# Kernel optimization log

Hardware: AMD Instinct MI355X
Metric: run time of the kernel (lower is better)

Reference implementation:

```python
import jax, jax.numpy as jnp
import numpy as np

N = 50000      # nodes
E = 400000     # edges (avg degree 8)
IN = 512       # in_dim
HID = 512      # hid
NUM_RSU = 1000 # batch==0 nodes; equals max(batch)+1 so cat() row counts match


def setup_inputs() -> dict:
    key = jax.random.key(0)
    ks = jax.random.split(key, 5)
    x = jax.random.normal(ks[0], (N, IN), jnp.float32)
    edge_index = jax.random.randint(ks[1], (2, E), 0, N, jnp.int32)
    # sorted graph ids: first NUM_RSU nodes are RSU (batch 0), rest split into 999 vehicle graphs
    n_veh = N - NUM_RSU
    veh_batch = 1 + (jnp.arange(n_veh) * (NUM_RSU - 1)) // n_veh
    batch = jnp.concatenate([jnp.zeros(NUM_RSU, jnp.int32), veh_batch.astype(jnp.int32)])
    W1 = jax.random.normal(ks[2], (IN, HID), jnp.float32) * (1.0 / np.sqrt(IN))
    b1 = jnp.zeros((HID,), jnp.float32)
    W2 = jax.random.normal(ks[3], (HID, HID), jnp.float32) * (1.0 / np.sqrt(HID))
    b2 = jnp.zeros((HID,), jnp.float32)
    return {"x": x, "edge_index": edge_index, "batch": batch,
            "W1": W1, "b1": b1, "W2": W2, "b2": b2, "num_rsu": NUM_RSU}


def reference(x, edge_index, batch, W1, b1, W2, b2, num_rsu):
    n = x.shape[0]
    loop = jnp.arange(n, dtype=edge_index.dtype)
    src = jnp.concatenate([edge_index[0], loop])  # self-loops appended (GCNConv default)
    dst = jnp.concatenate([edge_index[1], loop])
    # symmetric normalization D^{-1/2} (A+I) D^{-1/2}
    deg = jax.ops.segment_sum(jnp.ones_like(dst, jnp.float32), dst, num_segments=n)
    dinv = jnp.where(deg > 0, jax.lax.rsqrt(deg), 0.0)
    norm = dinv[src] * dinv[dst]  # [E+N]

    def gcn(h, W, b):
        m = (h @ W)[src] * norm[:, None]                       # gather + scale
        return jax.ops.segment_sum(m, dst, num_segments=n) + b # scatter-add

    h = jax.nn.relu(gcn(x, W1, b1))
    h = gcn(h, W2, b2)

    rsu = h[:num_rsu]                 # batch == 0 nodes (sorted layout)
    veh = h[num_rsu:]
    seg = batch[num_rsu:]             # values 1..num_rsu-1
    s = jax.ops.segment_sum(veh, seg, num_segments=num_rsu)
    cnt = jax.ops.segment_sum(jnp.ones_like(seg, jnp.float32), seg, num_segments=num_rsu)
    veh_pool = s / jnp.maximum(cnt, 1.0)[:, None]  # mean pool; empty segment 0 stays zero
    return jnp.concatenate([rsu, veh_pool], axis=-1)
```

## Files before the change

### kernel.cpp

```cpp
#include <hip/hip_runtime.h>

#define N_NODES 50000
#define E_EDGES 400000
#define DIM     512
#define NRSU    1000
#define NVEH    (N_NODES - NRSU)
#define NB_SCAN 196

typedef __attribute__((ext_vector_type(8))) __bf16 bf16x8;
typedef __attribute__((ext_vector_type(4))) float  f32x4;
typedef __attribute__((ext_vector_type(8))) unsigned short ush8v;

__device__ __forceinline__ unsigned short f2bf_rne(float x) {
    unsigned u = __float_as_uint(x);
    unsigned r = u + 0x7fff + ((u >> 16) & 1);
    return (unsigned short)(r >> 16);
}
__device__ __forceinline__ float bf2f(unsigned short b) {
    return __uint_as_float((unsigned)b << 16);
}
__device__ __forceinline__ void split1(float v, unsigned short& h, unsigned short& l) {
    h = f2bf_rne(v);
    l = f2bf_rne(v - bf2f(h));
}
__device__ __forceinline__ void cvt8(uint4 v, float* f) {
    f[0] = __uint_as_float(v.x << 16); f[1] = __uint_as_float(v.x & 0xffff0000u);
    f[2] = __uint_as_float(v.y << 16); f[3] = __uint_as_float(v.y & 0xffff0000u);
    f[4] = __uint_as_float(v.z << 16); f[5] = __uint_as_float(v.z & 0xffff0000u);
    f[6] = __uint_as_float(v.w << 16); f[7] = __uint_as_float(v.w & 0xffff0000u);
}

typedef __attribute__((address_space(1))) const unsigned char ga_u8;
typedef __attribute__((address_space(3))) unsigned char la_u8;
__device__ __forceinline__ void gload16(const void* g, void* l) {
    __builtin_amdgcn_global_load_lds((ga_u8*)g, (la_u8*)l, 16, 0, 0);
}

__global__ void k_zero_int(int* __restrict__ p, int n) {
    int i = blockIdx.x * 256 + threadIdx.x;
    if (i < n) p[i] = 0;
}

__global__ void k_tobf16(const float* __restrict__ in, unsigned short* __restrict__ out) {
    size_t i = ((size_t)blockIdx.x * 256 + threadIdx.x) * 8;
    float4 a = *reinterpret_cast<const float4*>(in + i);
    float4 b = *reinterpret_cast<const float4*>(in + i + 4);
    ush8v o;
    o[0] = f2bf_rne(a.x); o[1] = f2bf_rne(a.y); o[2] = f2bf_rne(a.z); o[3] = f2bf_rne(a.w);
    o[4] = f2bf_rne(b.x); o[5] = f2bf_rne(b.y); o[6] = f2bf_rne(b.z); o[7] = f2bf_rne(b.w);
    *reinterpret_cast<ush8v*>(out + i) = o;
}

__global__ void k_count(const int* __restrict__ dst, int* __restrict__ cnt) {
    int e = blockIdx.x * 256 + threadIdx.x;
    if (e < E_EDGES) atomicAdd(&cnt[dst[e]], 1);
}

__global__ __launch_bounds__(256) void k_scan1(const int* __restrict__ cnt,
                                               int* __restrict__ rowptr,
                                               int* __restrict__ bsum) {
    __shared__ int sh[256];
    int tid = threadIdx.x;
    int i = blockIdx.x * 256 + tid;
    int v = (i < N_NODES) ? cnt[i] : 0;
    sh[tid] = v;
    __syncthreads();
    #pragma unroll
    for (int off = 1; off < 256; off <<= 1) {
        int t = (tid >= off) ? sh[tid - off] : 0;
        __syncthreads();
        sh[tid] += t;
        __syncthreads();
    }
    if (i < N_NODES) rowptr[i] = sh[tid] - v;
    if (tid == 255) bsum[blockIdx.x] = sh[255];
}

__global__ __launch_bounds__(256) void k_scan2(int* __restrict__ bsum) {
    __shared__ int sh[256];
    int tid = threadIdx.x;
    int v = (tid < NB_SCAN) ? bsum[tid] : 0;
    sh[tid] = v;
    __syncthreads();
    #pragma unroll
    for (int off = 1; off < 256; off <<= 1) {
        int t = (tid >= off) ? sh[tid - off] : 0;
        __syncthreads();
        sh[tid] += t;
        __syncthreads();
    }
    if (tid < NB_SCAN) bsum[tid] = sh[tid] - v;
}

__global__ void k_scan3(int* __restrict__ rowptr, const int* __restrict__ bsum,
                        int* __restrict__ cntfill, float* __restrict__ dinv) {
    int i = blockIdx.x * 256 + threadIdx.x;
    if (i < N_NODES) {
        rowptr[i] += bsum[blockIdx.x];
        int c = cntfill[i];
        dinv[i] = rsqrtf((float)c + 1.0f);
        cntfill[i] = 0;
    }
    if (i == 0) rowptr[N_NODES] = E_EDGES;
}

__global__ void k_fill(const int* __restrict__ ei, const int* __restrict__ rowptr,
                       int* __restrict__ fill, int* __restrict__ col,
                       const float* __restrict__ dinv, float* __restrict__ wnorm) {
    int e = blockIdx.x * 256 + threadIdx.x;
    if (e >= E_EDGES) return;
    int s = ei[e];
    int d = ei[E_EDGES + e];
    int p = atomicAdd(&fill[d], 1);
    int idx = rowptr[d] + p;
    col[idx] = s;
    wnorm[idx] = dinv[s] * dinv[d];
}

__global__ void k_segbounds(const int* __restrict__ batch, int* __restrict__ seg) {
    int v = blockIdx.x * 256 + threadIdx.x;
    if (v >= NVEH) return;
    int b = batch[NRSU + v];
    if (v == 0) {
        for (int s = 0; s <= b; ++s) seg[s] = 0;
    } else {
        int bp = batch[NRSU + v - 1];
        for (int s = bp + 1; s <= b; ++s) seg[s] = v;
    }
    if (v == NVEH - 1) {
        for (int s = b + 1; s <= NRSU; ++s) seg[s] = NVEH;
    }
}

__global__ void k_wsplit(const float* __restrict__ W1, const float* __restrict__ W2,
                         unsigned short* __restrict__ W1h, unsigned short* __restrict__ W1l,
                         unsigned short* __restrict__ W2h, unsigned short* __restrict__ W2l) {
    const float* W = blockIdx.y ? W2 : W1;
    unsigned short* Wh = blockIdx.y ? W2h : W1h;
    unsigned short* Wl = blockIdx.y ? W2l : W1l;
    int n = blockIdx.x;
    for (int k = threadIdx.x; k < DIM; k += 256) {
        float v = W[(size_t)k * DIM + n];
        unsigned short h, l;
        split1(v, h, l);
        Wh[(size_t)n * DIM + k] = h;
        Wl[(size_t)n * DIM + k] = l;
    }
}

template<int MODE>
__global__ __launch_bounds__(256) void k_gemm_mfma(const unsigned short* __restrict__ Ab,
                                                   const unsigned short* __restrict__ BhT,
                                                   const unsigned short* __restrict__ BlT,
                                                   float* __restrict__ C,
                                                   unsigned short* __restrict__ Cb, int M,
                                                   const float* __restrict__ bias,
                                                   const float* __restrict__ bscale) {
    const int BM = 128, BN = 128, BK = 32;
    __shared__ unsigned short sA [BM * BK];
    __shared__ unsigned short sBh[BN * BK];
    __shared__ unsigned short sBl[BN * BK];

    int tid = threadIdx.x;
    int wv = tid >> 6;
    int ln = tid & 63;

    int wgid;
    if (MODE == 2) {
        const int q = 195, r = 4;
        int id = blockIdx.x;
        int xcd = id & 7, idx = id >> 3;
        wgid = (xcd < r ? xcd * (q + 1) : r * (q + 1) + (xcd - r) * q) + idx;
    } else {
        wgid = blockIdx.x;
    }
    int col0 = (wgid & 3) * BN;
    int row0 = (wgid >> 2) * BM;

    int wr = wv >> 1, wc = wv & 1;
    int fr = ln & 15;
    int ks16 = ln >> 4;

    f32x4 zero = {0.f, 0.f, 0.f, 0.f};
    f32x4 acc[4][4];
    #pragma unroll
    for (int m = 0; m < 4; ++m)
        #pragma unroll
        for (int n = 0; n < 4; ++n) acc[m][n] = zero;

    for (int k0 = 0; k0 < DIM; k0 += BK) {
        __syncthreads();
        #pragma unroll
        for (int p = 0; p < 2; ++p) {
            int idx = p * 256 + tid;
            int r = idx >> 2;
            int slot = idx & 3;
            int c = ((slot ^ ((r >> 1) & 3)) << 3);
            int arow = row0 + r; if (arow > M - 1) arow = M - 1;
            size_t aoff = (size_t)arow * DIM + k0 + c;
            size_t boff = (size_t)(col0 + r) * DIM + k0 + c;
            int lbyte = p * 4096 + wv * 1024;
            gload16(Ab + aoff, (char*)sA + lbyte);
            gload16(BhT + boff, (char*)sBh + lbyte);
            gload16(BlT + boff, (char*)sBl + lbyte);
        }
        __syncthreads();

        bf16x8 a[4], bh[4], bl[4];
        #pragma unroll
        for (int m = 0; m < 4; ++m) {
            int r = wr * 64 + m * 16 + fr;
            int e = r * BK + ((ks16 ^ ((r >> 1) & 3)) << 3);
            a[m] = *reinterpret_cast<const bf16x8*>(&sA[e]);
        }
        #pragma unroll
        for (int n = 0; n < 4; ++n) {
            int r = wc * 64 + n * 16 + fr;
            int e = r * BK + ((ks16 ^ ((r >> 1) & 3)) << 3);
            bh[n] = *reinterpret_cast<const bf16x8*>(&sBh[e]);
            bl[n] = *reinterpret_cast<const bf16x8*>(&sBl[e]);
        }
        #pragma unroll
        for (int m = 0; m < 4; ++m)
            #pragma unroll
            for (int n = 0; n < 4; ++n) {
                acc[m][n] = __builtin_amdgcn_mfma_f32_16x16x32_bf16(a[m], bh[n], acc[m][n], 0, 0, 0);
                acc[m][n] = __builtin_amdgcn_mfma_f32_16x16x32_bf16(a[m], bl[n], acc[m][n], 0, 0, 0);
            }
    }

    int rbase = row0 + wr * 64 + (ln >> 4) * 4;
    int cbase = col0 + wc * 64 + (ln & 15);
    #pragma unroll
    for (int m = 0; m < 4; ++m)
        #pragma unroll
        for (int r4 = 0; r4 < 4; ++r4) {
            int row = rbase + m * 16 + r4;
            if (row < M) {
                if (MODE == 2) {
                    #pragma unroll
                    for (int n = 0; n < 4; ++n) {
                        int cc = cbase + n * 16;
                        Cb[(size_t)row * DIM + cc] =
                            f2bf_rne(fmaxf(acc[m][n][r4] + bias[cc], 0.f));
                    }
                } else {
                    float bs = bscale[row];
                    float* dst = (row < NRSU) ? (C + (size_t)row * 1024)
                                              : (C + (size_t)(row - NRSU) * 1024 + 512);
                    #pragma unroll
                    for (int n = 0; n < 4; ++n) {
                        int cc = cbase + n * 16;
                        dst[cc] = acc[m][n][r4] + bias[cc] * bs;
                    }
                }
            }
        }
}

__global__ __launch_bounds__(256) void k_gather_bf(const int* __restrict__ rowptr,
                                                   const int* __restrict__ col,
                                                   const float* __restrict__ wnorm,
                                                   const float* __restrict__ dinv,
                                                   const unsigned short* __restrict__ pre,
                                                   unsigned short* __restrict__ ob) {
    int node = blockIdx.x * 4 + (threadIdx.x >> 6);
    if (node >= N_NODES) return;
    int lane = threadIdx.x & 63;
    int c = lane * 8;

    float di = dinv[node];
    float w0 = di * di;
    float s[8], t[8];
    {
        uint4 sv = *reinterpret_cast<const uint4*>(pre + (size_t)node * DIM + c);
        float fa[8]; cvt8(sv, fa);
        #pragma unroll
        for (int i = 0; i < 8; ++i) { s[i] = w0 * fa[i]; t[i] = 0.f; }
    }

    int beg = rowptr[node], end = rowptr[node + 1];
    int deg = end - beg;
    for (int j0 = 0; j0 < deg; j0 += 64) {
        int j = j0 + lane;
        int cj = 0; float wj = 0.f;
        if (j < deg) { cj = col[beg + j]; wj = wnorm[beg + j]; }
        int lim = deg - j0; if (lim > 64) lim = 64;
        for (int jj = 0; jj < lim; jj += 8) {
            int sidx[8]; float sw[8];
            #pragma unroll
            for (int q = 0; q < 8; ++q) {
                sidx[q] = __shfl(cj, jj + q);
                sw[q]   = __shfl(wj, jj + q);
            }
            uint4 v[8];
            #pragma unroll
            for (int q = 0; q < 8; ++q)
                v[q] = *reinterpret_cast<const uint4*>(pre + (size_t)sidx[q] * DIM + c);
            #pragma unroll
            for (int q = 0; q < 8; ++q) {
                float f[8]; cvt8(v[q], f);
                if ((q & 1) == 0) {
                    #pragma unroll
                    for (int i = 0; i < 8; ++i) s[i] = fmaf(sw[q], f[i], s[i]);
                } else {
                    #pragma unroll
                    for (int i = 0; i < 8; ++i) t[i] = fmaf(sw[q], f[i], t[i]);
                }
            }
        }
    }
    ush8v h;
    #pragma unroll
    for (int i = 0; i < 8; ++i) h[i] = f2bf_rne(s[i] + t[i]);
    *reinterpret_cast<ush8v*>(ob + (size_t)node * DIM + c) = h;
}

__global__ __launch_bounds__(64) void k_pool_sp(const unsigned short* __restrict__ A2b,
                                                const int* __restrict__ seg,
                                                unsigned short* __restrict__ SPb,
                                                float* __restrict__ bscale) {
    int s = blockIdx.x;
    int c = threadIdx.x * 8;
    {
        uint4 v = *reinterpret_cast<const uint4*>(A2b + (size_t)s * DIM + c);
        *reinterpret_cast<uint4*>(SPb + (size_t)s * DIM + c) = v;
    }
    int beg = seg[s], end = seg[s + 1];
    float acc[8] = {0.f, 0.f, 0.f, 0.f, 0.f, 0.f, 0.f, 0.f};
    for (int v = beg; v < end; ++v) {
        uint4 t = *reinterpret_cast<const uint4*>(A2b + (size_t)(NRSU + v) * DIM + c);
        float f[8]; cvt8(t, f);
        #pragma unroll
        for (int i = 0; i < 8; ++i) acc[i] += f[i];
    }
    float inv = 1.0f / fmaxf((float)(end - beg), 1.0f);
    ush8v h;
    #pragma unroll
    for (int i = 0; i < 8; ++i) h[i] = f2bf_rne(acc[i] * inv);
    *reinterpret_cast<ush8v*>(SPb + (size_t)(NRSU + s) * DIM + c) = h;
    if (threadIdx.x == 0) {
        bscale[s] = 1.0f;
        bscale[NRSU + s] = (end > beg) ? 1.0f : 0.0f;
    }
}

extern "C" void kernel_launch(void* const* d_in, const int* in_sizes, int n_in,
                              void* d_out, int out_size, void* d_ws, size_t ws_size,
                              hipStream_t stream) {
    const float* x     = (const float*)d_in[0];
    const int*   ei    = (const int*)d_in[1];
    const int*   batch = (const int*)d_in[2];
    const float* W1    = (const float*)d_in[3];
    const float* b1    = (const float*)d_in[4];
    const float* W2    = (const float*)d_in[5];
    const float* b2    = (const float*)d_in[6];
    float* out = (float*)d_out;

    char* ws = (char*)d_ws;
    const size_t HALF = (size_t)N_NODES * DIM * 2;
    unsigned short* Axb = (unsigned short*)(ws);
    unsigned short* A2b = (unsigned short*)(ws);
    unsigned short* h1b = (unsigned short*)(ws + 2 * HALF);
    unsigned short* xb  = (unsigned short*)(ws + 3 * HALF);
    char* p = ws + 4 * HALF;
    float* dinv    = (float*)p;                p += (size_t)N_NODES * 4;
    int*   cnt     = (int*)p;                  p += (size_t)N_NODES * 4;
    int*   rowptr  = (int*)p;                  p += (size_t)(N_NODES + 4) * 4;
    int*   col     = (int*)p;                  p += (size_t)E_EDGES * 4;
    float* wnorm   = (float*)p;                p += (size_t)E_EDGES * 4;
    int*   bsum    = (int*)p;                  p += 1024;
    int*   seg     = (int*)p;                  p += (size_t)(NRSU + 8) * 4;
    unsigned short* SPb = (unsigned short*)p;  p += (size_t)2 * NRSU * DIM * 2;
    float* bscale  = (float*)p;                p += (size_t)2 * NRSU * 4;
    unsigned short* W1h = (unsigned short*)p;  p += (size_t)DIM * DIM * 2;
    unsigned short* W1l = (unsigned short*)p;  p += (size_t)DIM * DIM * 2;
    unsigned short* W2h = (unsigned short*)p;  p += (size_t)DIM * DIM * 2;
    unsigned short* W2l = (unsigned short*)p;  p += (size_t)DIM * DIM * 2;

    dim3 blk(256);
    const int gN = (N_NODES + 255) / 256;
    const int gE = (E_EDGES + 255) / 256;
    const int gV = (NVEH + 255) / 256;

    k_zero_int <<<gN, blk, 0, stream>>>(cnt, N_NODES);
    k_count    <<<gE, blk, 0, stream>>>(ei + E_EDGES, cnt);
    k_scan1    <<<gN, blk, 0, stream>>>(cnt, rowptr, bsum);
    k_scan2    <<<1,  blk, 0, stream>>>(bsum);
    k_scan3    <<<gN, blk, 0, stream>>>(rowptr, bsum, cnt, dinv);
    k_fill     <<<gE, blk, 0, stream>>>(ei, rowptr, cnt, col, dinv, wnorm);
    k_segbounds<<<gV, blk, 0, stream>>>(batch, seg);
    k_wsplit   <<<dim3(DIM, 2), blk, 0, stream>>>(W1, W2, W1h, W1l, W2h, W2l);
    k_tobf16   <<<(int)((size_t)N_NODES * DIM / 8 / 256), blk, 0, stream>>>(x, xb);

    k_gather_bf<<<(N_NODES + 3) / 4, blk, 0, stream>>>(rowptr, col, wnorm, dinv, xb, Axb);
    const int NWG1 = ((N_NODES + 127) / 128) * 4;
    k_gemm_mfma<2><<<NWG1, blk, 0, stream>>>(Axb, W1h, W1l, nullptr, h1b, N_NODES, b1, nullptr);

    k_gather_bf<<<(N_NODES + 3) / 4, blk, 0, stream>>>(rowptr, col, wnorm, dinv, h1b, A2b);
    k_pool_sp<<<NRSU, dim3(64), 0, stream>>>(A2b, seg, SPb, bscale);
    const int NWG2 = ((2 * NRSU + 127) / 128) * 4;
    k_gemm_mfma<1><<<NWG2, blk, 0, stream>>>(SPb, W2h, W2l, out, nullptr, 2 * NRSU, b2, bscale);
}
```

Baseline: 354.8 us.

## Load GEMM MFMA operands directly from global memory instead of staging through LDS

The bf16 split-precision GEMM no longer stages A and B tiles into shared memory with global_load_lds and barriers. Each lane now reads its MFMA fragments straight from global memory through precomputed row pointers, and the k-loop is unrolled by 4. This removes the two __syncthreads per k-step and the LDS round trip. In exchange, operands are no longer shared across waves, so each wave re-reads tiles from global or L2 memory, and the loads are strided 16-byte reads that coalesce less well.

```diff
diff --git a/kernel.cpp b/kernel.cpp
--- a/kernel.cpp
+++ b/kernel.cpp
@@ -28,12 +28,6 @@
     f[2] = __uint_as_float(v.y << 16); f[3] = __uint_as_float(v.y & 0xffff0000u);
     f[4] = __uint_as_float(v.z << 16); f[5] = __uint_as_float(v.z & 0xffff0000u);
     f[6] = __uint_as_float(v.w << 16); f[7] = __uint_as_float(v.w & 0xffff0000u);
-}
-
-typedef __attribute__((address_space(1))) const unsigned char ga_u8;
-typedef __attribute__((address_space(3))) unsigned char la_u8;
-__device__ __forceinline__ void gload16(const void* g, void* l) {
-    __builtin_amdgcn_global_load_lds((ga_u8*)g, (la_u8*)l, 16, 0, 0);
 }
 
 __global__ void k_zero_int(int* __restrict__ p, int n) {
@@ -156,11 +150,7 @@
                                                    unsigned short* __restrict__ Cb, int M,
                                                    const float* __restrict__ bias,
                                                    const float* __restrict__ bscale) {
-    const int BM = 128, BN = 128, BK = 32;
-    __shared__ unsigned short sA [BM * BK];
-    __shared__ unsigned short sBh[BN * BK];
-    __shared__ unsigned short sBl[BN * BK];
-
+    const int BM = 128, BN = 128;
     int tid = threadIdx.x;
     int wv = tid >> 6;
     int ln = tid & 63;
@@ -181,6 +171,22 @@
     int fr = ln & 15;
     int ks16 = ln >> 4;
 
+    const unsigned short* ap[4];
+    const unsigned short* bhp[4];
+    const unsigned short* blp[4];
+    #pragma unroll
+    for (int m = 0; m < 4; ++m) {
+        int row = row0 + wr * 64 + m * 16 + fr;
+        if (row > M - 1) row = M - 1;
+        ap[m] = Ab + (size_t)row * DIM + ks16 * 8;
+    }
+    #pragma unroll
+    for (int n = 0; n < 4; ++n) {
+        int r = col0 + wc * 64 + n * 16 + fr;
+        bhp[n] = BhT + (size_t)r * DIM + ks16 * 8;
+        blp[n] = BlT + (size_t)r * DIM + ks16 * 8;
+    }
+
     f32x4 zero = {0.f, 0.f, 0.f, 0.f};
     f32x4 acc[4][4];
     #pragma unroll
@@ -188,37 +194,16 @@
         #pragma unroll
         for (int n = 0; n < 4; ++n) acc[m][n] = zero;
 
-    for (int k0 = 0; k0 < DIM; k0 += BK) {
-        __syncthreads();
-        #pragma unroll
-        for (int p = 0; p < 2; ++p) {
-            int idx = p * 256 + tid;
-            int r = idx >> 2;
-            int slot = idx & 3;
-            int c = ((slot ^ ((r >> 1) & 3)) << 3);
-            int arow = row0 + r; if (arow > M - 1) arow = M - 1;
-            size_t aoff = (size_t)arow * DIM + k0 + c;
-            size_t boff = (size_t)(col0 + r) * DIM + k0 + c;
-            int lbyte = p * 4096 + wv * 1024;
-            gload16(Ab + aoff, (char*)sA + lbyte);
-            gload16(BhT + boff, (char*)sBh + lbyte);
-            gload16(BlT + boff, (char*)sBl + lbyte);
-        }
-        __syncthreads();
-
+    #pragma unroll 4
+    for (int k0 = 0; k0 < DIM; k0 += 32) {
         bf16x8 a[4], bh[4], bl[4];
         #pragma unroll
-        for (int m = 0; m < 4; ++m) {
-            int r = wr * 64 + m * 16 + fr;
-            int e = r * BK + ((ks16 ^ ((r >> 1) & 3)) << 3);
-            a[m] = *reinterpret_cast<const bf16x8*>(&sA[e]);
-        }
+        for (int m = 0; m < 4; ++m)
+            a[m] = *reinterpret_cast<const bf16x8*>(ap[m] + k0);
         #pragma unroll
         for (int n = 0; n < 4; ++n) {
-            int r = wc * 64 + n * 16 + fr;
-            int e = r * BK + ((ks16 ^ ((r >> 1) & 3)) << 3);
-            bh[n] = *reinterpret_cast<const bf16x8*>(&sBh[e]);
-            bl[n] = *reinterpret_cast<const bf16x8*>(&sBl[e]);
+            bh[n] = *reinterpret_cast<const bf16x8*>(bhp[n] + k0);
+            bl[n] = *reinterpret_cast<const bf16x8*>(blp[n] + k0);
         }
         #pragma unroll
         for (int m = 0; m < 4; ++m)
```

After: 432.8 us. 1.22x slower.

## Drop bf16 hi/lo weight split and double-buffer GEMM LDS tiles

Applied to the files above, without the earlier changes.

Weights are now converted to a single bf16 copy instead of a hi/lo pair, which halves the MFMA count and the B-tile loads in both GEMMs. The GEMM main loop also gains double-buffered LDS with prefetch of the next K tile and precomputed global pointers, aiming to overlap loads with MFMA work. The cost is lower accuracy in the weight operand, since the low-order correction term is gone, so the error against the fp32 reference grows.

```diff
diff --git a/kernel.cpp b/kernel.cpp
--- a/kernel.cpp
+++ b/kernel.cpp
@@ -18,10 +18,6 @@
 }
 __device__ __forceinline__ float bf2f(unsigned short b) {
     return __uint_as_float((unsigned)b << 16);
-}
-__device__ __forceinline__ void split1(float v, unsigned short& h, unsigned short& l) {
-    h = f2bf_rne(v);
-    l = f2bf_rne(v - bf2f(h));
 }
 __device__ __forceinline__ void cvt8(uint4 v, float* f) {
     f[0] = __uint_as_float(v.x << 16); f[1] = __uint_as_float(v.x & 0xffff0000u);
@@ -132,34 +128,26 @@
     }
 }
 
-__global__ void k_wsplit(const float* __restrict__ W1, const float* __restrict__ W2,
-                         unsigned short* __restrict__ W1h, unsigned short* __restrict__ W1l,
-                         unsigned short* __restrict__ W2h, unsigned short* __restrict__ W2l) {
+__global__ void k_wT(const float* __restrict__ W1, const float* __restrict__ W2,
+                     unsigned short* __restrict__ W1T, unsigned short* __restrict__ W2T) {
     const float* W = blockIdx.y ? W2 : W1;
-    unsigned short* Wh = blockIdx.y ? W2h : W1h;
-    unsigned short* Wl = blockIdx.y ? W2l : W1l;
+    unsigned short* WT = blockIdx.y ? W2T : W1T;
     int n = blockIdx.x;
     for (int k = threadIdx.x; k < DIM; k += 256) {
-        float v = W[(size_t)k * DIM + n];
-        unsigned short h, l;
-        split1(v, h, l);
-        Wh[(size_t)n * DIM + k] = h;
-        Wl[(size_t)n * DIM + k] = l;
+        WT[(size_t)n * DIM + k] = f2bf_rne(W[(size_t)k * DIM + n]);
     }
 }
 
 template<int MODE>
 __global__ __launch_bounds__(256) void k_gemm_mfma(const unsigned short* __restrict__ Ab,
-                                                   const unsigned short* __restrict__ BhT,
-                                                   const unsigned short* __restrict__ BlT,
+                                                   const unsigned short* __restrict__ BT,
                                                    float* __restrict__ C,
                                                    unsigned short* __restrict__ Cb, int M,
                                                    const float* __restrict__ bias,
                                                    const float* __restrict__ bscale) {
-    const int BM = 128, BN = 128, BK = 32;
-    __shared__ unsigned short sA [BM * BK];
-    __shared__ unsigned short sBh[BN * BK];
-    __shared__ unsigned short sBl[BN * BK];
+    const int BM = 128, BN = 128, BK = 32, NT = DIM / BK;
+    __shared__ unsigned short sA[2][BM * BK];
+    __shared__ unsigned short sB[2][BN * BK];
 
     int tid = threadIdx.x;
     int wv = tid >> 6;
@@ -181,6 +169,20 @@
     int fr = ln & 15;
     int ks16 = ln >> 4;
 
+    int sidx0 = tid, sidx1 = 256 + tid;
+    int r0 = sidx0 >> 2, s0 = sidx0 & 3;
+    int r1 = sidx1 >> 2, s1 = sidx1 & 3;
+    int c0 = ((s0 ^ ((r0 >> 1) & 3)) << 3);
+    int c1 = ((s1 ^ ((r1 >> 1) & 3)) << 3);
+    int ar0 = row0 + r0; if (ar0 > M - 1) ar0 = M - 1;
+    int ar1 = row0 + r1; if (ar1 > M - 1) ar1 = M - 1;
+    const unsigned short* ga0 = Ab + (size_t)ar0 * DIM + c0;
+    const unsigned short* ga1 = Ab + (size_t)ar1 * DIM + c1;
+    const unsigned short* gb0 = BT + (size_t)(col0 + r0) * DIM + c0;
+    const unsigned short* gb1 = BT + (size_t)(col0 + r1) * DIM + c1;
+    int lb0 = wv * 1024;
+    int lb1 = 4096 + wv * 1024;
+
     f32x4 zero = {0.f, 0.f, 0.f, 0.f};
     f32x4 acc[4][4];
     #pragma unroll
@@ -188,45 +190,41 @@
         #pragma unroll
         for (int n = 0; n < 4; ++n) acc[m][n] = zero;
 
-    for (int k0 = 0; k0 < DIM; k0 += BK) {
-        __syncthreads();
-        #pragma unroll
-        for (int p = 0; p < 2; ++p) {
-            int idx = p * 256 + tid;
-            int r = idx >> 2;
-            int slot = idx & 3;
-            int c = ((slot ^ ((r >> 1) & 3)) << 3);
-            int arow = row0 + r; if (arow > M - 1) arow = M - 1;
-            size_t aoff = (size_t)arow * DIM + k0 + c;
-            size_t boff = (size_t)(col0 + r) * DIM + k0 + c;
-            int lbyte = p * 4096 + wv * 1024;
-            gload16(Ab + aoff, (char*)sA + lbyte);
-            gload16(BhT + boff, (char*)sBh + lbyte);
-            gload16(BlT + boff, (char*)sBl + lbyte);
+    gload16(ga0, (char*)sA[0] + lb0);
+    gload16(ga1, (char*)sA[0] + lb1);
+    gload16(gb0, (char*)sB[0] + lb0);
+    gload16(gb1, (char*)sB[0] + lb1);
+    __syncthreads();
+
+    #pragma unroll
+    for (int t = 0; t < NT; ++t) {
+        int cur = t & 1;
+        if (t + 1 < NT) {
+            int k0n = (t + 1) * BK;
+            gload16(ga0 + k0n, (char*)sA[cur ^ 1] + lb0);
+            gload16(ga1 + k0n, (char*)sA[cur ^ 1] + lb1);
+            gload16(gb0 + k0n, (char*)sB[cur ^ 1] + lb0);
+            gload16(gb1 + k0n, (char*)sB[cur ^ 1] + lb1);
         }
-        __syncthreads();
-
-        bf16x8 a[4], bh[4], bl[4];
+        bf16x8 a[4], b[4];
         #pragma unroll
         for (int m = 0; m < 4; ++m) {
             int r = wr * 64 + m * 16 + fr;
             int e = r * BK + ((ks16 ^ ((r >> 1) & 3)) << 3);
-            a[m] = *reinterpret_cast<const bf16x8*>(&sA[e]);
+            a[m] = *reinterpret_cast<const bf16x8*>(&sA[cur][e]);
         }
         #pragma unroll
         for (int n = 0; n < 4; ++n) {
             int r = wc * 64 + n * 16 + fr;
             int e = r * BK + ((ks16 ^ ((r >> 1) & 3)) << 3);
-            bh[n] = *reinterpret_cast<const bf16x8*>(&sBh[e]);
-            bl[n] = *reinterpret_cast<const bf16x8*>(&sBl[e]);
+            b[n] = *reinterpret_cast<const bf16x8*>(&sB[cur][e]);
         }
         #pragma unroll
         for (int m = 0; m < 4; ++m)
             #pragma unroll
-            for (int n = 0; n < 4; ++n) {
-                acc[m][n] = __builtin_amdgcn_mfma_f32_16x16x32_bf16(a[m], bh[n], acc[m][n], 0, 0, 0);
-                acc[m][n] = __builtin_amdgcn_mfma_f32_16x16x32_bf16(a[m], bl[n], acc[m][n], 0, 0, 0);
-            }
+            for (int n = 0; n < 4; ++n)
+                acc[m][n] = __builtin_amdgcn_mfma_f32_16x16x32_bf16(a[m], b[n], acc[m][n], 0, 0, 0);
+        __syncthreads();
     }
 
     int rbase = row0 + wr * 64 + (ln >> 4) * 4;
@@ -373,10 +371,8 @@
     int*   seg     = (int*)p;                  p += (size_t)(NRSU + 8) * 4;
     unsigned short* SPb = (unsigned short*)p;  p += (size_t)2 * NRSU * DIM * 2;
     float* bscale  = (float*)p;                p += (size_t)2 * NRSU * 4;
-    unsigned short* W1h = (unsigned short*)p;  p += (size_t)DIM * DIM * 2;
-    unsigned short* W1l = (unsigned short*)p;  p += (size_t)DIM * DIM * 2;
-    unsigned short* W2h = (unsigned short*)p;  p += (size_t)DIM * DIM * 2;
-    unsigned short* W2l = (unsigned short*)p;  p += (size_t)DIM * DIM * 2;
+    unsigned short* W1T = (unsigned short*)p;  p += (size_t)DIM * DIM * 2;
+    unsigned short* W2T = (unsigned short*)p;  p += (size_t)DIM * DIM * 2;
 
     dim3 blk(256);
     const int gN = (N_NODES + 255) / 256;
@@ -390,15 +386,15 @@
     k_scan3    <<<gN, blk, 0, stream>>>(rowptr, bsum, cnt, dinv);
     k_fill     <<<gE, blk, 0, stream>>>(ei, rowptr, cnt, col, dinv, wnorm);
     k_segbounds<<<gV, blk, 0, stream>>>(batch, seg);
-    k_wsplit   <<<dim3(DIM, 2), blk, 0, stream>>>(W1, W2, W1h, W1l, W2h, W2l);
+    k_wT       <<<dim3(DIM, 2), blk, 0, stream>>>(W1, W2, W1T, W2T);
     k_tobf16   <<<(int)((size_t)N_NODES * DIM / 8 / 256), blk, 0, stream>>>(x, xb);
 
     k_gather_bf<<<(N_NODES + 3) / 4, blk, 0, stream>>>(rowptr, col, wnorm, dinv, xb, Axb);
     const int NWG1 = ((N_NODES + 127) / 128) * 4;
-    k_gemm_mfma<2><<<NWG1, blk, 0, stream>>>(Axb, W1h, W1l, nullptr, h1b, N_NODES, b1, nullptr);
+    k_gemm_mfma<2><<<NWG1, blk, 0, stream>>>(Axb, W1T, nullptr, h1b, N_NODES, b1, nullptr);
 
     k_gather_bf<<<(N_NODES + 3) / 4, blk, 0, stream>>>(rowptr, col, wnorm, dinv, h1b, A2b);
     k_pool_sp<<<NRSU, dim3(64), 0, stream>>>(A2b, seg, SPb, bscale);
     const int NWG2 = ((2 * NRSU + 127) / 128) * 4;
-    k_gemm_mfma<1><<<NWG2, blk, 0, stream>>>(SPb, W2h, W2l, out, nullptr, 2 * NRSU, b2, bscale);
-}
+    k_gemm_mfma<1><<<NWG2, blk, 0, stream>>>(SPb, W2T, out, nullptr, 2 * NRSU, b2, bscale);
+}
```

After: 309.2 us. -12.8%, faster.
